# Optimization experiments

Hardware: AMD Instinct MI355X
Metric: run time of the kernel (lower is better)

Reference implementation:

```python
import jax, jax.numpy as jnp
import numpy as np
from functools import partial

D = 1024
H = 4 * D
E = 8
K_TOP = 2
B, T = 4, 2048
NEG_INF = jnp.float32(-1e30)


def setup_inputs() -> dict:
    key = jax.random.key(0)
    ks = jax.random.split(key, 12)
    s = 0.02
    return {
        "x": jax.random.normal(ks[0], (B, T, D), jnp.float32),
        "noise": jax.random.normal(ks[1], (B, T, E), jnp.float32),
        "gate_w": jax.random.normal(ks[2], (E, D), jnp.float32) * s,
        "gate_b": jnp.zeros((E,), jnp.float32),
        "var_w": jax.random.normal(ks[3], (E, D), jnp.float32) * s,
        "var_b": jnp.zeros((E,), jnp.float32),
        "w1": jax.random.normal(ks[4], (E, H, D), jnp.float32) * s,
        "b1": jnp.zeros((E, H), jnp.float32),
        "w2": jax.random.normal(ks[5], (E, D, H), jnp.float32) * s,
        "b2": jnp.zeros((E, D), jnp.float32),
    }


def reference(x, noise, gate_w, gate_b, var_w, var_b, w1, b1, w2, b2):
    # Noisy top-k gating
    logits = jnp.einsum("btd,ed->bte", x, gate_w) + gate_b          # [B,T,E]
    std = jax.nn.softplus(jnp.einsum("btd,ed->bte", x, var_w) + var_b)
    noisy = logits + noise * std                                      # [B,T,E]
    _, idx = jax.lax.top_k(noisy, K_TOP)                              # [B,T,K]
    # boolean top-k mask over experts
    mask = (idx[..., None] == jnp.arange(E)).any(axis=-2)             # [B,T,E]
    coef = jax.nn.softmax(jnp.where(mask, noisy, NEG_INF), axis=-1)   # zeros outside top-k

    # Combine: sum_e coef_e * FFN_e(x). coef is exactly 0 for non-selected
    # experts, so this equals the masked gather/scatter math. Scan over the
    # small expert dim to avoid a [E,B,T,H] intermediate.
    coef_e = jnp.moveaxis(coef, -1, 0)                                # [E,B,T]

    def body(acc, ew):
        w1e, b1e, w2e, b2e, ce = ew
        h = jax.nn.relu(jnp.einsum("btd,hd->bth", x, w1e) + b1e)
        y = jnp.einsum("bth,dh->btd", h, w2e) + b2e
        return acc + y * ce[..., None], None

    out, _ = jax.lax.scan(body, jnp.zeros_like(x), (w1, b1, w2, b2, coef_e))
    return out
```

## Files before the change

kernel.cpp:

```cpp
#include <hip/hip_runtime.h>
#include <hip/hip_bf16.h>
#include <math.h>

#define NTOK 8192
#define DD   1024
#define HH   4096
#define NE   8
#define BM 128
#define BN 128
#define BK 64
#define SLOT_CAP (2 * NTOK + NE * BM)

typedef __bf16 bf16;
typedef __bf16 bf16x8 __attribute__((ext_vector_type(8)));
typedef __bf16 bf16x4 __attribute__((ext_vector_type(4)));
typedef float  f32x4  __attribute__((ext_vector_type(4)));

typedef __attribute__((address_space(3))) unsigned char lds_u8;
typedef const __attribute__((address_space(1))) unsigned char g_u8;

__device__ __forceinline__ void gload16(const bf16* g, bf16* l) {
  __builtin_amdgcn_global_load_lds((g_u8*)g, (lds_u8*)l, 16, 0, 0);
}

__device__ __forceinline__ float softplus_f(float v) {
  return fmaxf(v, 0.f) + log1pf(expf(-fabsf(v)));
}

__global__ __launch_bounds__(64) void moe_gate_kernel(
    const float* __restrict__ x, const float* __restrict__ noise,
    const float* __restrict__ gate_w, const float* __restrict__ gate_b,
    const float* __restrict__ var_w,  const float* __restrict__ var_b,
    float* __restrict__ coef2, int* __restrict__ t2e, int* __restrict__ counts,
    bf16* __restrict__ xb)
{
  const int lane = threadIdx.x;
  const float4* gw4 = (const float4*)gate_w;
  const float4* vw4 = (const float4*)var_w;
  for (int tt = 0; tt < 16; ++tt) {
    const int t = blockIdx.x * 16 + tt;
    const float4* x4 = (const float4*)(x + (size_t)t * DD);
    bf16x4* xb4 = (bf16x4*)(xb + (size_t)t * DD);
    float pg[NE], pv[NE];
    #pragma unroll
    for (int e = 0; e < NE; ++e) { pg[e] = 0.f; pv[e] = 0.f; }
    #pragma unroll
    for (int i = 0; i < DD / 256; ++i) {
      const int d4 = i * 64 + lane;
      const float4 f = x4[d4];
      bf16x4 v;
      v[0] = (bf16)f.x; v[1] = (bf16)f.y; v[2] = (bf16)f.z; v[3] = (bf16)f.w;
      xb4[d4] = v;
      #pragma unroll
      for (int e = 0; e < NE; ++e) {
        const float4 g = gw4[e * 256 + d4];
        pg[e] = fmaf(f.x, g.x, fmaf(f.y, g.y, fmaf(f.z, g.z, fmaf(f.w, g.w, pg[e]))));
        const float4 w = vw4[e * 256 + d4];
        pv[e] = fmaf(f.x, w.x, fmaf(f.y, w.y, fmaf(f.z, w.z, fmaf(f.w, w.w, pv[e]))));
      }
    }
    #pragma unroll
    for (int e = 0; e < NE; ++e) {
      #pragma unroll
      for (int off = 32; off; off >>= 1) {
        pg[e] += __shfl_xor(pg[e], off);
        pv[e] += __shfl_xor(pv[e], off);
      }
    }
    if (lane == 0) {
      float noisy[NE];
      #pragma unroll
      for (int e = 0; e < NE; ++e) {
        const float lg = pg[e] + gate_b[e];
        const float sd = softplus_f(pv[e] + var_b[e]);
        noisy[e] = lg + noise[t * NE + e] * sd;
      }
      int i1 = 0; float n1 = noisy[0];
      #pragma unroll
      for (int e = 1; e < NE; ++e) if (noisy[e] > n1) { n1 = noisy[e]; i1 = e; }
      int i2 = -1; float n2 = -3.0e38f;
      #pragma unroll
      for (int e = 0; e < NE; ++e) if (e != i1 && noisy[e] > n2) { n2 = noisy[e]; i2 = e; }
      const float e2 = expf(n2 - n1);
      const float den = 1.f + e2;
      coef2[t * 2 + 0] = 1.f / den;
      coef2[t * 2 + 1] = e2 / den;
      t2e[t * 2 + 0] = i1;
      t2e[t * 2 + 1] = i2;
      atomicAdd(&counts[i1], 1);
      atomicAdd(&counts[i2], 1);
    }
  }
}

__global__ void moe_offsets_kernel(const int* __restrict__ counts, int* __restrict__ po) {
  if (threadIdx.x == 0) {
    int acc = 0;
    po[0] = 0;
    for (int e = 0; e < NE; ++e) {
      acc += ((counts[e] + BM - 1) / BM) * BM;
      po[e + 1] = acc;
    }
  }
}

__global__ __launch_bounds__(256) void moe_scatter_kernel(
    const int* __restrict__ t2e, const float* __restrict__ coef2,
    const int* __restrict__ po, int* __restrict__ cnt2,
    int* __restrict__ assign_tok, float* __restrict__ slot_coef)
{
  const int t = blockIdx.x * 256 + threadIdx.x;
  if (t >= NTOK) return;
  #pragma unroll
  for (int k = 0; k < 2; ++k) {
    const int e = t2e[t * 2 + k];
    const int pos = atomicAdd(&cnt2[e], 1);
    const int slot = po[e] + pos;
    assign_tok[slot] = t;
    slot_coef[slot] = coef2[t * 2 + k];
  }
}

__global__ __launch_bounds__(256) void cvt2_bf16_kernel(
    const float* __restrict__ s1, bf16* __restrict__ d1, int n41,
    const float* __restrict__ s2, bf16* __restrict__ d2, int n42)
{
  for (int i = blockIdx.x * 256 + threadIdx.x; i < n41 + n42; i += gridDim.x * 256) {
    const float* s = (i < n41) ? s1 : s2;
    bf16* d = (i < n41) ? d1 : d2;
    const int j = (i < n41) ? i : i - n41;
    const float4 f = ((const float4*)s)[j];
    bf16x4 v;
    v[0] = (bf16)f.x; v[1] = (bf16)f.y; v[2] = (bf16)f.z; v[3] = (bf16)f.w;
    ((bf16x4*)d)[j] = v;
  }
}

template<int KDIM, int NCOLS, bool FFN1>
__global__ __launch_bounds__(256) void moe_gemm_kernel(
    const bf16* __restrict__ Asrc, const bf16* __restrict__ Wsrc,
    const float* __restrict__ bias,
    const int* __restrict__ assign_tok, const float* __restrict__ slot_coef,
    const int* __restrict__ po,
    bf16* __restrict__ hout, float* __restrict__ out,
    int chunk_base, int gx)
{
  __shared__ bf16 As[BM][BK];
  __shared__ bf16 Bs[BN][BK];
  __shared__ int toks[BM];

  const int nwg = gridDim.x;
  const int lin = blockIdx.x;
  const int q = nwg >> 3, r = nwg & 7;
  const int xcd = lin & 7, idx = lin >> 3;
  const int wg = (xcd < r ? xcd * (q + 1) : r * (q + 1) + (xcd - r) * q) + idx;
  int bx, by;
  if constexpr (FFN1) { bx = wg % gx; by = wg / gx; }
  else               { by = wg % (NCOLS / BN); bx = wg / (NCOLS / BN); }

  const int po8 = po[NE];
  const int row0 = chunk_base + bx * BM;
  if (row0 >= po8) return;
  int e = 0;
  while (row0 >= po[e + 1]) ++e;
  const int bn0 = by * BN;
  const bf16* We = Wsrc + (size_t)e * ((size_t)HH * DD);
  const int tid = threadIdx.x, lane = tid & 63, wave = tid >> 6;
  if (tid < BM) toks[tid] = assign_tok[row0 + tid];
  __syncthreads();

  const int rin = lane >> 3;
  const int c8s = (lane & 7) * 8;
  const bf16* asrc[4];
  const bf16* bsrc[4];
  #pragma unroll
  for (int i = 0; i < 4; ++i) {
    const int row = (wave * 4 + i) * 8 + rin;
    int ar;
    if constexpr (FFN1) {
      const int s = toks[row];
      ar = s < 0 ? 0 : s;
    } else {
      ar = row0 - chunk_base + row;
    }
    asrc[i] = Asrc + (size_t)ar * KDIM + c8s;
    bsrc[i] = We + (size_t)(bn0 + row) * KDIM + c8s;
  }

  const int la = lane & 15, hi = lane >> 4;
  const int wm = (wave >> 1) * 64, wn = (wave & 1) * 64;
  f32x4 acc[4][4];
  #pragma unroll
  for (int m = 0; m < 4; ++m)
    #pragma unroll
    for (int n = 0; n < 4; ++n) acc[m][n] = {0.f, 0.f, 0.f, 0.f};

  for (int k0 = 0; k0 < KDIM; k0 += BK) {
    #pragma unroll
    for (int i = 0; i < 4; ++i) gload16(asrc[i] + k0, &As[(wave * 4 + i) * 8][0]);
    #pragma unroll
    for (int i = 0; i < 4; ++i) gload16(bsrc[i] + k0, &Bs[(wave * 4 + i) * 8][0]);
    __syncthreads();
    #pragma unroll
    for (int ks = 0; ks < 2; ++ks) {
      bf16x8 af[4], bff[4];
      #pragma unroll
      for (int m = 0; m < 4; ++m)
        af[m] = *(const bf16x8*)(&As[wm + m * 16 + la][ks * 32 + hi * 8]);
      #pragma unroll
      for (int n = 0; n < 4; ++n)
        bff[n] = *(const bf16x8*)(&Bs[wn + n * 16 + la][ks * 32 + hi * 8]);
      #pragma unroll
      for (int m = 0; m < 4; ++m)
        #pragma unroll
        for (int n = 0; n < 4; ++n)
          acc[m][n] = __builtin_amdgcn_mfma_f32_16x16x32_bf16(af[m], bff[n], acc[m][n], 0, 0, 0);
    }
    __syncthreads();
  }

  if constexpr (FFN1) {
    const int hrow0 = row0 - chunk_base;
    #pragma unroll
    for (int n = 0; n < 4; ++n) {
      const int col = bn0 + wn + n * 16 + la;
      const float bb = bias[e * NCOLS + col];
      #pragma unroll
      for (int m = 0; m < 4; ++m) {
        const int rbase = wm + m * 16 + hi * 4;
        #pragma unroll
        for (int rr = 0; rr < 4; ++rr) {
          float v = acc[m][n][rr] + bb;
          v = v > 0.f ? v : 0.f;
          hout[(size_t)(hrow0 + rbase + rr) * HH + col] = (bf16)v;
        }
      }
    }
  } else {
    #pragma unroll
    for (int n = 0; n < 4; ++n) {
      const int col = bn0 + wn + n * 16 + la;
      const float bb = bias[e * NCOLS + col];
      #pragma unroll
      for (int m = 0; m < 4; ++m) {
        const int rbase = wm + m * 16 + hi * 4;
        #pragma unroll
        for (int rr = 0; rr < 4; ++rr) {
          const int trow = rbase + rr;
          const int tok = toks[trow];
          if (tok >= 0) {
            const float c = slot_coef[row0 + trow];
            atomicAdd(out + (size_t)tok * DD + col, c * (acc[m][n][rr] + bb));
          }
        }
      }
    }
  }
}

extern "C" void kernel_launch(void* const* d_in, const int* in_sizes, int n_in,
                              void* d_out, int out_size, void* d_ws, size_t ws_size,
                              hipStream_t stream) {
  const float* x      = (const float*)d_in[0];
  const float* noise  = (const float*)d_in[1];
  const float* gate_w = (const float*)d_in[2];
  const float* gate_b = (const float*)d_in[3];
  const float* var_w  = (const float*)d_in[4];
  const float* var_b  = (const float*)d_in[5];
  const float* w1     = (const float*)d_in[6];
  const float* b1     = (const float*)d_in[7];
  const float* w2     = (const float*)d_in[8];
  const float* b2     = (const float*)d_in[9];
  float* out = (float*)d_out;
  (void)in_sizes; (void)n_in; (void)out_size;

  char* ws = (char*)d_ws;
  size_t off = 0;
  auto alloc = [&](size_t bytes) {
    off = (off + 255) & ~(size_t)255;
    size_t o = off;
    off += bytes;
    return o;
  };
  bf16*  xb         = (bf16*)(ws + alloc((size_t)NTOK * DD * 2));
  float* coef2      = (float*)(ws + alloc((size_t)NTOK * 2 * 4));
  int*   t2e        = (int*)(ws + alloc((size_t)NTOK * 2 * 4));
  int*   counts     = (int*)(ws + alloc(64));
  int*   cnt2       = counts + 8;
  int*   po         = (int*)(ws + alloc(64));
  int*   assign_tok = (int*)(ws + alloc((size_t)SLOT_CAP * 4));
  float* slot_coef  = (float*)(ws + alloc((size_t)SLOT_CAP * 4));
  bf16*  w1b        = (bf16*)(ws + alloc((size_t)NE * HH * DD * 2));
  bf16*  w2b        = (bf16*)(ws + alloc((size_t)NE * DD * HH * 2));
  off = (off + 255) & ~(size_t)255;
  const size_t h_avail = ws_size > off ? ws_size - off : 0;
  int chunk_rows = (int)(h_avail / ((size_t)HH * 2));
  chunk_rows = (chunk_rows / BM) * BM;
  if (chunk_rows < BM) chunk_rows = BM;
  if (chunk_rows > SLOT_CAP) chunk_rows = SLOT_CAP;
  bf16* hbuf = (bf16*)(ws + off);

  hipMemsetAsync(counts, 0, 64, stream);
  hipMemsetAsync(assign_tok, 0xFF, (size_t)SLOT_CAP * 4, stream);
  hipMemsetAsync(out, 0, (size_t)NTOK * DD * 4, stream);

  moe_gate_kernel<<<NTOK / 16, 64, 0, stream>>>(x, noise, gate_w, gate_b, var_w, var_b,
                                                coef2, t2e, counts, xb);
  moe_offsets_kernel<<<1, 64, 0, stream>>>(counts, po);
  moe_scatter_kernel<<<NTOK / 256, 256, 0, stream>>>(t2e, coef2, po, cnt2,
                                                     assign_tok, slot_coef);
  cvt2_bf16_kernel<<<2048, 256, 0, stream>>>(w1, w1b, NE * HH * DD / 4,
                                             w2, w2b, NE * DD * HH / 4);

  const int rounds = (SLOT_CAP + chunk_rows - 1) / chunk_rows;
  for (int r = 0; r < rounds; ++r) {
    const int cb = r * chunk_rows;
    const int rows_here = (cb + chunk_rows <= SLOT_CAP) ? chunk_rows : (SLOT_CAP - cb);
    const int gx = rows_here / BM;
    moe_gemm_kernel<DD, HH, true><<<gx * (HH / BN), 256, 0, stream>>>(
        xb, w1b, b1, assign_tok, slot_coef, po, hbuf, nullptr, cb, gx);
    moe_gemm_kernel<HH, DD, false><<<gx * (DD / BN), 256, 0, stream>>>(
        hbuf, w2b, b2, assign_tok, slot_coef, po, nullptr, out, cb, gx);
  }
}
```

Before: 1.008 ms.

## Make MoE GEMMs persistent over a fixed grid and XOR-swizzle LDS tiles

Both expert GEMM launches now use a fixed grid of 1024 workgroups. Each workgroup loops over its XCD-local slice of output tiles, where before there was one workgroup per tile. The LDS layout of the A and B tiles is XOR-swizzled by row so that column chunks are permuted, which is meant to cut LDS bank conflicts on the fragment reads. The persistent loop avoids launching and early-exiting many empty tiles, but it adds extra barriers per tile and may unbalance work across workgroups.

```diff
diff --git a/kernel.cpp b/kernel.cpp
--- a/kernel.cpp
+++ b/kernel.cpp
@@ -10,6 +10,7 @@
 #define BN 128
 #define BK 64
 #define SLOT_CAP (2 * NTOK + NE * BM)
+#define PERS 1024
 
 typedef __bf16 bf16;
 typedef __bf16 bf16x8 __attribute__((ext_vector_type(8)));
@@ -143,114 +144,125 @@
     const int* __restrict__ assign_tok, const float* __restrict__ slot_coef,
     const int* __restrict__ po,
     bf16* __restrict__ hout, float* __restrict__ out,
-    int chunk_base, int gx)
+    int chunk_base, int gx, int nwg)
 {
   __shared__ bf16 As[BM][BK];
   __shared__ bf16 Bs[BN][BK];
   __shared__ int toks[BM];
 
-  const int nwg = gridDim.x;
-  const int lin = blockIdx.x;
+  const int p = blockIdx.x;
   const int q = nwg >> 3, r = nwg & 7;
-  const int xcd = lin & 7, idx = lin >> 3;
-  const int wg = (xcd < r ? xcd * (q + 1) : r * (q + 1) + (xcd - r) * q) + idx;
-  int bx, by;
-  if constexpr (FFN1) { bx = wg % gx; by = wg / gx; }
-  else               { by = wg % (NCOLS / BN); bx = wg / (NCOLS / BN); }
-
+  const int xc = p & 7;
+  const int sx = xc < r ? q + 1 : q;
+  const int s0 = xc < r ? xc * (q + 1) : r * (q + 1) + (xc - r) * q;
+  const int tid = threadIdx.x, lane = tid & 63, wave = tid >> 6;
   const int po8 = po[NE];
-  const int row0 = chunk_base + bx * BM;
-  if (row0 >= po8) return;
-  int e = 0;
-  while (row0 >= po[e + 1]) ++e;
-  const int bn0 = by * BN;
-  const bf16* We = Wsrc + (size_t)e * ((size_t)HH * DD);
-  const int tid = threadIdx.x, lane = tid & 63, wave = tid >> 6;
-  if (tid < BM) toks[tid] = assign_tok[row0 + tid];
-  __syncthreads();
-
   const int rin = lane >> 3;
-  const int c8s = (lane & 7) * 8;
-  const bf16* asrc[4];
-  const bf16* bsrc[4];
-  #pragma unroll
-  for (int i = 0; i < 4; ++i) {
-    const int row = (wave * 4 + i) * 8 + rin;
-    int ar;
-    if constexpr (FFN1) {
-      const int s = toks[row];
-      ar = s < 0 ? 0 : s;
-    } else {
-      ar = row0 - chunk_base + row;
-    }
-    asrc[i] = Asrc + (size_t)ar * KDIM + c8s;
-    bsrc[i] = We + (size_t)(bn0 + row) * KDIM + c8s;
-  }
-
+  const int c8s = ((lane & 7) ^ rin) * 8;
   const int la = lane & 15, hi = lane >> 4;
   const int wm = (wave >> 1) * 64, wn = (wave & 1) * 64;
-  f32x4 acc[4][4];
-  #pragma unroll
-  for (int m = 0; m < 4; ++m)
-    #pragma unroll
-    for (int n = 0; n < 4; ++n) acc[m][n] = {0.f, 0.f, 0.f, 0.f};
-
-  for (int k0 = 0; k0 < KDIM; k0 += BK) {
-    #pragma unroll
-    for (int i = 0; i < 4; ++i) gload16(asrc[i] + k0, &As[(wave * 4 + i) * 8][0]);
-    #pragma unroll
-    for (int i = 0; i < 4; ++i) gload16(bsrc[i] + k0, &Bs[(wave * 4 + i) * 8][0]);
+
+  for (int it = p >> 3; it < sx; it += PERS / 8) {
+    const int wg = s0 + it;
+    int bx, by;
+    if constexpr (FFN1) { bx = wg % gx; by = wg / gx; }
+    else               { by = wg % (NCOLS / BN); bx = wg / (NCOLS / BN); }
+    const int row0 = chunk_base + bx * BM;
+    if (row0 >= po8) continue;
+    int e = 0;
+    while (row0 >= po[e + 1]) ++e;
+    const int bn0 = by * BN;
+    const bf16* We = Wsrc + (size_t)e * ((size_t)HH * DD);
+
     __syncthreads();
-    #pragma unroll
-    for (int ks = 0; ks < 2; ++ks) {
-      bf16x8 af[4], bff[4];
-      #pragma unroll
-      for (int m = 0; m < 4; ++m)
-        af[m] = *(const bf16x8*)(&As[wm + m * 16 + la][ks * 32 + hi * 8]);
-      #pragma unroll
-      for (int n = 0; n < 4; ++n)
-        bff[n] = *(const bf16x8*)(&Bs[wn + n * 16 + la][ks * 32 + hi * 8]);
-      #pragma unroll
-      for (int m = 0; m < 4; ++m)
-        #pragma unroll
-        for (int n = 0; n < 4; ++n)
-          acc[m][n] = __builtin_amdgcn_mfma_f32_16x16x32_bf16(af[m], bff[n], acc[m][n], 0, 0, 0);
-    }
+    if (tid < BM) toks[tid] = assign_tok[row0 + tid];
     __syncthreads();
-  }
-
-  if constexpr (FFN1) {
-    const int hrow0 = row0 - chunk_base;
-    #pragma unroll
-    for (int n = 0; n < 4; ++n) {
-      const int col = bn0 + wn + n * 16 + la;
-      const float bb = bias[e * NCOLS + col];
-      #pragma unroll
-      for (int m = 0; m < 4; ++m) {
-        const int rbase = wm + m * 16 + hi * 4;
-        #pragma unroll
-        for (int rr = 0; rr < 4; ++rr) {
-          float v = acc[m][n][rr] + bb;
-          v = v > 0.f ? v : 0.f;
-          hout[(size_t)(hrow0 + rbase + rr) * HH + col] = (bf16)v;
+
+    const bf16* asrc[4];
+    const bf16* bsrc[4];
+    #pragma unroll
+    for (int i = 0; i < 4; ++i) {
+      const int row = (wave * 4 + i) * 8 + rin;
+      int ar;
+      if constexpr (FFN1) {
+        const int s = toks[row];
+        ar = s < 0 ? 0 : s;
+      } else {
+        ar = row0 - chunk_base + row;
+      }
+      asrc[i] = Asrc + (size_t)ar * KDIM + c8s;
+      bsrc[i] = We + (size_t)(bn0 + row) * KDIM + c8s;
+    }
+
+    f32x4 acc[4][4];
+    #pragma unroll
+    for (int m = 0; m < 4; ++m)
+      #pragma unroll
+      for (int n = 0; n < 4; ++n) acc[m][n] = {0.f, 0.f, 0.f, 0.f};
+
+    for (int k0 = 0; k0 < KDIM; k0 += BK) {
+      #pragma unroll
+      for (int i = 0; i < 4; ++i) gload16(asrc[i] + k0, &As[(wave * 4 + i) * 8][0]);
+      #pragma unroll
+      for (int i = 0; i < 4; ++i) gload16(bsrc[i] + k0, &Bs[(wave * 4 + i) * 8][0]);
+      __syncthreads();
+      #pragma unroll
+      for (int ks = 0; ks < 2; ++ks) {
+        bf16x8 af[4], bff[4];
+        #pragma unroll
+        for (int m = 0; m < 4; ++m) {
+          const int row = wm + m * 16 + la;
+          const int c8 = (ks * 4 + hi) ^ (row & 7);
+          af[m] = *(const bf16x8*)(&As[row][c8 * 8]);
         }
-      }
-    }
-  } else {
-    #pragma unroll
-    for (int n = 0; n < 4; ++n) {
-      const int col = bn0 + wn + n * 16 + la;
-      const float bb = bias[e * NCOLS + col];
-      #pragma unroll
-      for (int m = 0; m < 4; ++m) {
-        const int rbase = wm + m * 16 + hi * 4;
-        #pragma unroll
-        for (int rr = 0; rr < 4; ++rr) {
-          const int trow = rbase + rr;
-          const int tok = toks[trow];
-          if (tok >= 0) {
-            const float c = slot_coef[row0 + trow];
-            atomicAdd(out + (size_t)tok * DD + col, c * (acc[m][n][rr] + bb));
+        #pragma unroll
+        for (int n = 0; n < 4; ++n) {
+          const int row = wn + n * 16 + la;
+          const int c8 = (ks * 4 + hi) ^ (row & 7);
+          bff[n] = *(const bf16x8*)(&Bs[row][c8 * 8]);
+        }
+        #pragma unroll
+        for (int m = 0; m < 4; ++m)
+          #pragma unroll
+          for (int n = 0; n < 4; ++n)
+            acc[m][n] = __builtin_amdgcn_mfma_f32_16x16x32_bf16(af[m], bff[n], acc[m][n], 0, 0, 0);
+      }
+      __syncthreads();
+    }
+
+    if constexpr (FFN1) {
+      const int hrow0 = row0 - chunk_base;
+      #pragma unroll
+      for (int n = 0; n < 4; ++n) {
+        const int col = bn0 + wn + n * 16 + la;
+        const float bb = bias[e * NCOLS + col];
+        #pragma unroll
+        for (int m = 0; m < 4; ++m) {
+          const int rbase = wm + m * 16 + hi * 4;
+          #pragma unroll
+          for (int rr = 0; rr < 4; ++rr) {
+            float v = acc[m][n][rr] + bb;
+            v = v > 0.f ? v : 0.f;
+            hout[(size_t)(hrow0 + rbase + rr) * HH + col] = (bf16)v;
+          }
+        }
+      }
+    } else {
+      #pragma unroll
+      for (int n = 0; n < 4; ++n) {
+        const int col = bn0 + wn + n * 16 + la;
+        const float bb = bias[e * NCOLS + col];
+        #pragma unroll
+        for (int m = 0; m < 4; ++m) {
+          const int rbase = wm + m * 16 + hi * 4;
+          #pragma unroll
+          for (int rr = 0; rr < 4; ++rr) {
+            const int trow = rbase + rr;
+            const int tok = toks[trow];
+            if (tok >= 0) {
+              const float c = slot_coef[row0 + trow];
+              atomicAdd(out + (size_t)tok * DD + col, c * (acc[m][n][rr] + bb));
+            }
           }
         }
       }
@@ -317,9 +329,9 @@
     const int cb = r * chunk_rows;
     const int rows_here = (cb + chunk_rows <= SLOT_CAP) ? chunk_rows : (SLOT_CAP - cb);
     const int gx = rows_here / BM;
-    moe_gemm_kernel<DD, HH, true><<<gx * (HH / BN), 256, 0, stream>>>(
-        xb, w1b, b1, assign_tok, slot_coef, po, hbuf, nullptr, cb, gx);
-    moe_gemm_kernel<HH, DD, false><<<gx * (DD / BN), 256, 0, stream>>>(
-        hbuf, w2b, b2, assign_tok, slot_coef, po, nullptr, out, cb, gx);
-  }
-}
+    moe_gemm_kernel<DD, HH, true><<<PERS, 256, 0, stream>>>(
+        xb, w1b, b1, assign_tok, slot_coef, po, hbuf, nullptr, cb, gx, gx * (HH / BN));
+    moe_gemm_kernel<HH, DD, false><<<PERS, 256, 0, stream>>>(
+        hbuf, w2b, b2, assign_tok, slot_coef, po, nullptr, out, cb, gx, gx * (DD / BN));
+  }
+}
```

New measurement: 919.6 us. -8.7%, faster.
